# Kernel optimization log

Hardware: AMD Instinct MI355X
Metric: run time of the kernel (lower is better)

## Reference

```python
import jax, jax.numpy as jnp
import numpy as np

B, T, E, D = 64, 512, 1024, 1024  # batch, enc timesteps, enc hidden, dec hidden


def setup_inputs() -> dict:
    key = jax.random.key(0)
    ks = jax.random.split(key, 9)
    s = lambda fan_in: 1.0 / np.sqrt(fan_in)
    return {
        "hidden": jax.random.normal(ks[0], (B, D), jnp.float32),
        "decoder_out": jax.random.normal(ks[1], (B, D), jnp.float32),
        "encoder_states": jax.random.normal(ks[2], (T, B, E), jnp.float32),
        # attn: Linear(D+E -> 2E)
        "Wa": jax.random.uniform(ks[3], (2 * E, D + E), jnp.float32, -s(D + E), s(D + E)),
        "ba": jax.random.uniform(ks[4], (2 * E,), jnp.float32, -s(D + E), s(D + E)),
        # attn2: Linear(2E -> 1)
        "w2": jax.random.uniform(ks[5], (1, 2 * E), jnp.float32, -s(2 * E), s(2 * E)),
        "b2": jax.random.uniform(ks[6], (1,), jnp.float32, -s(2 * E), s(2 * E)),
        # attn_combine: Linear(D+E -> D)
        "Wc": jax.random.uniform(ks[7], (D, D + E), jnp.float32, -s(D + E), s(D + E)),
        "bc": jax.random.uniform(ks[8], (D,), jnp.float32, -s(D + E), s(D + E)),
    }


def reference(hidden, decoder_out, encoder_states, Wa, ba, w2, b2, Wc, bc):
    d = hidden.shape[1]
    # attn(cat(hidden, enc_t)) = hidden @ Wa[:, :D].T + enc_t @ Wa[:, D:].T + ba
    h_proj = hidden @ Wa[:, :d].T + ba                      # [B, 2E]
    e_proj = jnp.einsum('tbe,fe->tbf', encoder_states, Wa[:, d:])  # [T, B, 2E]
    act = jnp.tanh(h_proj[None, :, :] + e_proj)             # [T, B, 2E]
    scores = jnp.einsum('tbf,f->bt', act, w2[0]) + b2[0]    # [B, T]
    weights = jax.nn.softmax(scores, axis=-1)               # softmax over timesteps
    # weighted sum of encoder states: [B, E]
    applied = jnp.einsum('bt,tbe->be', weights, encoder_states)
    combined = jnp.concatenate([decoder_out, applied], axis=1)  # [B, D+E]
    out = jnp.tanh(combined @ Wc.T + bc)                    # [B, D]
    return out, applied
```

## Files before the change

kernel.cpp:

```cpp
#include <hip/hip_runtime.h>
#include <hip/hip_bf16.h>

#define BB 64
#define TT 512
#define EE 1024
#define DD 1024
#define BK 64

typedef __attribute__((ext_vector_type(8))) short s16x8;
typedef __attribute__((ext_vector_type(4))) float f32x4;

#define AS1 __attribute__((address_space(1)))
#define AS3 __attribute__((address_space(3)))

__device__ __forceinline__ float bf2f(unsigned short u) {
    unsigned int x = ((unsigned int)u) << 16;
    return __builtin_bit_cast(float, x);
}
__device__ __forceinline__ unsigned short f2bf(float f) {
    unsigned int u = __builtin_bit_cast(unsigned int, f);
    u += 0x7FFF + ((u >> 16) & 1);
    return (unsigned short)(u >> 16);
}
__device__ __forceinline__ float tanh_fast(float x) {
    x = fminf(fmaxf(x, -15.f), 15.f);
    float e = __expf(2.f * x);
    return (e - 1.f) / (e + 1.f);
}

__device__ __forceinline__ int tile_slot(int row, int g) {
    return (row >> 4) * 128 + (g >> 2) * 64 + (g & 3) * 16 + (row & 15);
}

__global__ __launch_bounds__(256) void conv_encS_kernel(
    const float* __restrict__ enc, unsigned short* __restrict__ encS)
{
    __shared__ short tileL[1024 * 8];
    const int tm  = blockIdx.x;
    const int tk  = blockIdx.y;
    const int tid = threadIdx.x;

#pragma unroll
    for (int it = 0; it < 4; ++it) {
        int cidx = it * 256 + tid;
        int row  = cidx >> 3;
        int g    = cidx & 7;
        const float* src = enc + (size_t)(tm * 128 + row) * 1024 + tk * 64 + g * 8;
        float4 v0 = ((const float4*)src)[0];
        float4 v1 = ((const float4*)src)[1];
        short c[8];
        c[0] = (short)f2bf(v0.x); c[1] = (short)f2bf(v0.y);
        c[2] = (short)f2bf(v0.z); c[3] = (short)f2bf(v0.w);
        c[4] = (short)f2bf(v1.x); c[5] = (short)f2bf(v1.y);
        c[6] = (short)f2bf(v1.z); c[7] = (short)f2bf(v1.w);
        *(s16x8*)&tileL[tile_slot(row, g) * 8] = *(s16x8*)c;
    }
    __syncthreads();
    unsigned short* dst = encS + ((size_t)tm * 16 + tk) * 8192;
#pragma unroll
    for (int it = 0; it < 4; ++it) {
        int s = it * 256 + tid;
        *(s16x8*)&dst[s * 8] = *(const s16x8*)&tileL[s * 8];
    }
}

__global__ __launch_bounds__(256) void conv_waS_kernel(
    const float* __restrict__ Wa, unsigned short* __restrict__ WaS)
{
    __shared__ short tileL[1024 * 8];
    const int tn  = blockIdx.x;
    const int tk  = blockIdx.y;
    const int tid = threadIdx.x;

#pragma unroll
    for (int it = 0; it < 4; ++it) {
        int cidx = it * 256 + tid;
        int row  = cidx >> 3;
        int g    = cidx & 7;
        const float* src = Wa + (size_t)(tn * 128 + row) * 2048 + 1024 + tk * 64 + g * 8;
        float4 v0 = ((const float4*)src)[0];
        float4 v1 = ((const float4*)src)[1];
        short c[8];
        c[0] = (short)f2bf(v0.x); c[1] = (short)f2bf(v0.y);
        c[2] = (short)f2bf(v0.z); c[3] = (short)f2bf(v0.w);
        c[4] = (short)f2bf(v1.x); c[5] = (short)f2bf(v1.y);
        c[6] = (short)f2bf(v1.z); c[7] = (short)f2bf(v1.w);
        *(s16x8*)&tileL[tile_slot(row, g) * 8] = *(s16x8*)c;
    }
    __syncthreads();
    unsigned short* dst = WaS + ((size_t)tn * 16 + tk) * 8192;
#pragma unroll
    for (int it = 0; it < 4; ++it) {
        int s = it * 256 + tid;
        *(s16x8*)&dst[s * 8] = *(const s16x8*)&tileL[s * 8];
    }
}

__global__ __launch_bounds__(256) void hproj_kernel(
    const float* __restrict__ hidden,
    const float* __restrict__ Wa,
    const float* __restrict__ ba,
    float* __restrict__ hp)
{
    __shared__ float sW[8 * 1024];
    const int tid  = threadIdx.x;
    const int lane = tid & 63;
    const int wave = tid >> 6;
    const int f0   = blockIdx.x * 8;

#pragma unroll
    for (int i = 0; i < 8; ++i) {
        int idx = i * 256 + tid;
        int fi  = idx >> 8;
        int c4  = idx & 255;
        ((float4*)sW)[idx] = *(const float4*)(Wa + (size_t)(f0 + fi) * 2048 + c4 * 4);
    }
    __syncthreads();

    for (int bi = 0; bi < 16; ++bi) {
        int b = wave * 16 + bi;
        float h[16];
#pragma unroll
        for (int j = 0; j < 16; ++j) h[j] = hidden[b * 1024 + lane + 64 * j];
#pragma unroll
        for (int fi = 0; fi < 8; ++fi) {
            float s = 0.f;
#pragma unroll
            for (int j = 0; j < 16; ++j) s += h[j] * sW[fi * 1024 + lane + 64 * j];
#pragma unroll
            for (int m = 32; m; m >>= 1) s += __shfl_xor(s, m);
            if (lane == 0) hp[(f0 + fi) * 64 + b] = s + ba[f0 + fi];
        }
    }
}

__global__ __launch_bounds__(512, 2) void gemm_scores(
    const unsigned short* __restrict__ encS,
    const unsigned short* __restrict__ WaS,
    const float* __restrict__ hp,
    const float* __restrict__ w2,
    float* __restrict__ scores)
{
    __shared__ short sA[2][2][8192];
    __shared__ short sB[2][2][8192];
    __shared__ float rowAcc[256];

    const int tid  = threadIdx.x;
    const int bid  = blockIdx.x;
    const int w    = (bid & 7) * 128 + (bid >> 3);
    const int bm   = w >> 3;
    const int bn   = w & 7;
    const int lane = tid & 63;
    const int wave = tid >> 6;
    const int wm   = wave >> 2;
    const int wn   = wave & 3;
    const int c    = lane & 15;
    const int quad = lane >> 4;
    const int ntile = wn >> 1;
    const int nrow0 = (wn & 1) * 4;

    f32x4 acc[8][4];
#pragma unroll
    for (int m = 0; m < 8; ++m)
#pragma unroll
        for (int n = 0; n < 4; ++n)
#pragma unroll
            for (int r = 0; r < 4; ++r) acc[m][n][r] = 0.f;

    const unsigned short* aT = encS + ((size_t)(bm * 2) * 16) * 8192;
    const unsigned short* bT = WaS  + ((size_t)(bn * 2) * 16) * 8192;

    auto STAGE_PAIR = [&](int kt, int nb, int p) {
        if (p < 2) {
            const unsigned short* src = aT + ((size_t)(p * 16 + kt)) * 8192;
            __builtin_amdgcn_global_load_lds(
                (const AS1 void*)(src + tid * 8),
                (AS3 void*)&sA[nb][p][tid * 8], 16, 0, 0);
            __builtin_amdgcn_global_load_lds(
                (const AS1 void*)(src + (512 + tid) * 8),
                (AS3 void*)&sA[nb][p][(512 + tid) * 8], 16, 0, 0);
        } else {
            const int nt = p - 2;
            const unsigned short* src = bT + ((size_t)(nt * 16 + kt)) * 8192;
            __builtin_amdgcn_global_load_lds(
                (const AS1 void*)(src + tid * 8),
                (AS3 void*)&sB[nb][nt][tid * 8], 16, 0, 0);
            __builtin_amdgcn_global_load_lds(
                (const AS1 void*)(src + (512 + tid) * 8),
                (AS3 void*)&sB[nb][nt][(512 + tid) * 8], 16, 0, 0);
        }
    };

#pragma unroll
    for (int p = 0; p < 4; ++p) STAGE_PAIR(0, 0, p);

    for (int kt = 0; kt < 16; ++kt) {
        const int cur = kt & 1;
        asm volatile("s_waitcnt vmcnt(0)" ::: "memory");
        __builtin_amdgcn_s_barrier();
        __builtin_amdgcn_sched_barrier(0);
        const bool pf = (kt < 15);

        s16x8 bF[2][4];
#pragma unroll
        for (int p = 0; p < 4; ++p) {
            if (p == 0) {
#pragma unroll
                for (int n = 0; n < 4; ++n)
#pragma unroll
                    for (int kk = 0; kk < 2; ++kk)
                        bF[kk][n] = *(const s16x8*)
                            &sB[cur][ntile][((nrow0 + n) * 128 + kk * 64 + lane) * 8];
            }
            s16x8 aF[2][2];
#pragma unroll
            for (int j = 0; j < 2; ++j)
#pragma unroll
                for (int kk = 0; kk < 2; ++kk)
                    aF[j][kk] = *(const s16x8*)
                        &sA[cur][wm][((2 * p + j) * 128 + kk * 64 + lane) * 8];

            if (pf) STAGE_PAIR(kt + 1, cur ^ 1, p);

            __builtin_amdgcn_sched_barrier(0);
            __builtin_amdgcn_s_barrier();
            __builtin_amdgcn_s_setprio(1);
#pragma unroll
            for (int j = 0; j < 2; ++j)
#pragma unroll
                for (int kk = 0; kk < 2; ++kk)
#pragma unroll
                    for (int n = 0; n < 4; ++n)
                        acc[2 * p + j][n] = __builtin_amdgcn_mfma_f32_16x16x32_bf16(
                            aF[j][kk], bF[kk][n], acc[2 * p + j][n], 0, 0, 0);
            __builtin_amdgcn_s_setprio(0);
            __builtin_amdgcn_sched_barrier(0);
            if (p < 3) __builtin_amdgcn_s_barrier();
        }
    }

    __syncthreads();
    if (tid < 256) rowAcc[tid] = 0.f;
    __syncthreads();

    float w2v[4];
#pragma unroll
    for (int n = 0; n < 4; ++n) w2v[n] = w2[bn * 256 + wn * 64 + n * 16 + c];

#pragma unroll
    for (int m = 0; m < 8; ++m) {
        int lrow0 = wm * 128 + m * 16 + quad * 4;
        int b0    = lrow0 & 63;
        f32x4 hp4[4];
#pragma unroll
        for (int n = 0; n < 4; ++n)
            hp4[n] = *(const f32x4*)&hp[(bn * 256 + wn * 64 + n * 16 + c) * 64 + b0];
#pragma unroll
        for (int r = 0; r < 4; ++r) {
            float s = 0.f;
#pragma unroll
            for (int n = 0; n < 4; ++n)
                s += tanh_fast(acc[m][n][r] + hp4[n][r]) * w2v[n];
            s += __shfl_xor(s, 1);
            s += __shfl_xor(s, 2);
            s += __shfl_xor(s, 4);
            s += __shfl_xor(s, 8);
            if (c == 0) atomicAdd(&rowAcc[lrow0 + r], s);
        }
    }
    __syncthreads();
    if (tid < 256) {
        int b = tid & 63;
        int t = bm * 4 + (tid >> 6);
        atomicAdd(&scores[b * TT + t], rowAcc[tid]);
    }
}

__global__ __launch_bounds__(256) void softmax_kernel(float* __restrict__ scores)
{
    __shared__ float wmax[4];
    __shared__ float wsum[4];
    const int b   = blockIdx.x;
    const int tid = threadIdx.x;
    float* row = scores + b * TT;

    float v0 = row[tid], v1 = row[tid + 256];
    float m = fmaxf(v0, v1);
#pragma unroll
    for (int s = 32; s; s >>= 1) m = fmaxf(m, __shfl_xor(m, s));
    if ((tid & 63) == 0) wmax[tid >> 6] = m;
    __syncthreads();
    m = fmaxf(fmaxf(wmax[0], wmax[1]), fmaxf(wmax[2], wmax[3]));

    float e0 = __expf(v0 - m), e1 = __expf(v1 - m);
    float s = e0 + e1;
#pragma unroll
    for (int t = 32; t; t >>= 1) s += __shfl_xor(s, t);
    if ((tid & 63) == 0) wsum[tid >> 6] = s;
    __syncthreads();
    float inv = 1.f / (wsum[0] + wsum[1] + wsum[2] + wsum[3]);
    row[tid]       = e0 * inv;
    row[tid + 256] = e1 * inv;
}

__global__ __launch_bounds__(256) void applied_part_kernel(
    const float* __restrict__ enc,
    const float* __restrict__ w,
    float* __restrict__ part)
{
    __shared__ float red[128 * 8];
    const int tc  = blockIdx.x;
    const int b   = blockIdx.y;
    const int tid = threadIdx.x;
    const int eo  = tid & 127;
    const int th  = tid >> 7;
    const int e0  = eo * 8;

    float a[8];
#pragma unroll
    for (int j = 0; j < 8; ++j) a[j] = 0.f;

    for (int it = 0; it < 16; ++it) {
        int t = tc * 32 + th * 16 + it;
        float wt = w[b * TT + t];
        const float* src = enc + ((size_t)(t * BB + b)) * EE + e0;
        float4 v0 = ((const float4*)src)[0];
        float4 v1 = ((const float4*)src)[1];
        a[0] += wt * v0.x; a[1] += wt * v0.y; a[2] += wt * v0.z; a[3] += wt * v0.w;
        a[4] += wt * v1.x; a[5] += wt * v1.y; a[6] += wt * v1.z; a[7] += wt * v1.w;
    }
    if (th == 1) {
#pragma unroll
        for (int j = 0; j < 8; ++j) red[eo * 8 + j] = a[j];
    }
    __syncthreads();
    if (th == 0) {
        float* dst = part + ((size_t)tc * 64 + b) * 1024 + e0;
#pragma unroll
        for (int j = 0; j < 8; ++j) dst[j] = a[j] + red[eo * 8 + j];
    }
}

__global__ __launch_bounds__(256) void applied_reduce_kernel(
    const float* __restrict__ part, float* __restrict__ out_applied)
{
    int idx = blockIdx.x * 256 + threadIdx.x;
    float s = 0.f;
#pragma unroll
    for (int tc = 0; tc < 16; ++tc) s += part[tc * 65536 + idx];
    out_applied[idx] = s;
}

__global__ __launch_bounds__(256) void combine_kernel(
    const float* __restrict__ dec,
    const float* applied,
    const float* __restrict__ Wc,
    const float* __restrict__ bc,
    float* out0)
{
    const int gw   = blockIdx.x * 4 + (threadIdx.x >> 6);
    const int lane = threadIdx.x & 63;
    const int d0   = (gw >> 3) * 8;
    const int b0   = (gw & 7) * 8;

    float acc[8][8];
#pragma unroll
    for (int dd = 0; dd < 8; ++dd)
#pragma unroll
        for (int bb = 0; bb < 8; ++bb) acc[dd][bb] = 0.f;

#pragma unroll
    for (int j = 0; j < 8; ++j) {
        float4 wv[8];
#pragma unroll
        for (int dd = 0; dd < 8; ++dd)
            wv[dd] = ((const float4*)(Wc + (size_t)(d0 + dd) * 2048))[j * 64 + lane];
        float4 cv[8];
        if (j < 4) {
#pragma unroll
            for (int bb = 0; bb < 8; ++bb)
                cv[bb] = ((const float4*)(dec + (size_t)(b0 + bb) * 1024))[j * 64 + lane];
        } else {
#pragma unroll
            for (int bb = 0; bb < 8; ++bb)
                cv[bb] = ((const float4*)(applied + (size_t)(b0 + bb) * 1024))[(j - 4) * 64 + lane];
        }
#pragma unroll
        for (int dd = 0; dd < 8; ++dd)
#pragma unroll
            for (int bb = 0; bb < 8; ++bb)
                acc[dd][bb] += wv[dd].x * cv[bb].x + wv[dd].y * cv[bb].y
                             + wv[dd].z * cv[bb].z + wv[dd].w * cv[bb].w;
    }

#pragma unroll
    for (int dd = 0; dd < 8; ++dd) {
#pragma unroll
        for (int bb = 0; bb < 8; ++bb) {
            float s = acc[dd][bb];
#pragma unroll
            for (int m = 32; m; m >>= 1) s += __shfl_xor(s, m);
            if (lane == 0)
                out0[(size_t)(b0 + bb) * DD + d0 + dd] = tanh_fast(s + bc[d0 + dd]);
        }
    }
}

extern "C" void kernel_launch(void* const* d_in, const int* in_sizes, int n_in,
                              void* d_out, int out_size, void* d_ws, size_t ws_size,
                              hipStream_t stream) {
    const float* hidden = (const float*)d_in[0];
    const float* dec    = (const float*)d_in[1];
    const float* enc    = (const float*)d_in[2];
    const float* Wa     = (const float*)d_in[3];
    const float* ba     = (const float*)d_in[4];
    const float* w2     = (const float*)d_in[5];
    const float* Wc     = (const float*)d_in[7];
    const float* bc     = (const float*)d_in[8];
    float* out = (float*)d_out;

    unsigned short* encS = (unsigned short*)d_ws;
    unsigned short* WaS  = encS + (size_t)33554432;
    float* hp     = (float*)(WaS + (size_t)2097152);
    float* scores = hp + 131072;
    float* part   = scores + 32768;

    hipMemsetAsync(scores, 0, BB * TT * sizeof(float), stream);
    dim3 gc(256, 16);
    conv_encS_kernel<<<gc, 256, 0, stream>>>(enc, encS);
    dim3 gw(16, 16);
    conv_waS_kernel<<<gw, 256, 0, stream>>>(Wa, WaS);
    hproj_kernel<<<256, 256, 0, stream>>>(hidden, Wa, ba, hp);
    gemm_scores<<<1024, 512, 0, stream>>>(encS, WaS, hp, w2, scores);
    softmax_kernel<<<BB, 256, 0, stream>>>(scores);
    dim3 g3(16, 64);
    applied_part_kernel<<<g3, 256, 0, stream>>>(enc, scores, part);
    applied_reduce_kernel<<<256, 256, 0, stream>>>(part, out + BB * DD);
    combine_kernel<<<256, 256, 0, stream>>>(dec, out + BB * DD, Wc, bc, out);
}
```

Before: 609.8 us.

## Use 1024-thread blocks in scores GEMM with 4x4 per-wave tiles

The scores GEMM now launches 16 waves per block instead of 8, so each wave owns a 64x64 sub-tile (4x4 MFMA accumulators) rather than 128x64. The per-phase staging/compute interleave with extra barriers is replaced by issuing the whole next-k prefetch at the start of each k-step, followed by two kk sub-steps of fragment loads and MFMAs. This halves accumulator registers per wave and cuts barrier count, aiming for more latency hiding. In exchange, each block has more waves contending for LDS, and occupancy drops to one block per CU, so overlap of loads with compute within a block becomes more important.

```diff
diff --git a/kernel.cpp b/kernel.cpp
--- a/kernel.cpp
+++ b/kernel.cpp
@@ -134,7 +134,7 @@
     }
 }
 
-__global__ __launch_bounds__(512, 2) void gemm_scores(
+__global__ __launch_bounds__(1024) void gemm_scores(
     const unsigned short* __restrict__ encS,
     const unsigned short* __restrict__ WaS,
     const float* __restrict__ hp,
@@ -156,12 +156,14 @@
     const int wn   = wave & 3;
     const int c    = lane & 15;
     const int quad = lane >> 4;
-    const int ntile = wn >> 1;
+    const int mt   = wm >> 1;
+    const int mrow0 = (wm & 1) * 4;
+    const int nt   = wn >> 1;
     const int nrow0 = (wn & 1) * 4;
 
-    f32x4 acc[8][4];
-#pragma unroll
-    for (int m = 0; m < 8; ++m)
+    f32x4 acc[4][4];
+#pragma unroll
+    for (int m = 0; m < 4; ++m)
 #pragma unroll
         for (int n = 0; n < 4; ++n)
 #pragma unroll
@@ -170,76 +172,54 @@
     const unsigned short* aT = encS + ((size_t)(bm * 2) * 16) * 8192;
     const unsigned short* bT = WaS  + ((size_t)(bn * 2) * 16) * 8192;
 
-    auto STAGE_PAIR = [&](int kt, int nb, int p) {
-        if (p < 2) {
-            const unsigned short* src = aT + ((size_t)(p * 16 + kt)) * 8192;
+    auto STAGE_ALL = [&](int kt, int nb) {
+#pragma unroll
+        for (int t = 0; t < 2; ++t) {
+            const unsigned short* sa = aT + ((size_t)(t * 16 + kt)) * 8192;
             __builtin_amdgcn_global_load_lds(
-                (const AS1 void*)(src + tid * 8),
-                (AS3 void*)&sA[nb][p][tid * 8], 16, 0, 0);
+                (const AS1 void*)(sa + tid * 8),
+                (AS3 void*)&sA[nb][t][tid * 8], 16, 0, 0);
+            const unsigned short* sb = bT + ((size_t)(t * 16 + kt)) * 8192;
             __builtin_amdgcn_global_load_lds(
-                (const AS1 void*)(src + (512 + tid) * 8),
-                (AS3 void*)&sA[nb][p][(512 + tid) * 8], 16, 0, 0);
-        } else {
-            const int nt = p - 2;
-            const unsigned short* src = bT + ((size_t)(nt * 16 + kt)) * 8192;
-            __builtin_amdgcn_global_load_lds(
-                (const AS1 void*)(src + tid * 8),
-                (AS3 void*)&sB[nb][nt][tid * 8], 16, 0, 0);
-            __builtin_amdgcn_global_load_lds(
-                (const AS1 void*)(src + (512 + tid) * 8),
-                (AS3 void*)&sB[nb][nt][(512 + tid) * 8], 16, 0, 0);
+                (const AS1 void*)(sb + tid * 8),
+                (AS3 void*)&sB[nb][t][tid * 8], 16, 0, 0);
         }
     };
 
-#pragma unroll
-    for (int p = 0; p < 4; ++p) STAGE_PAIR(0, 0, p);
+    STAGE_ALL(0, 0);
 
     for (int kt = 0; kt < 16; ++kt) {
         const int cur = kt & 1;
         asm volatile("s_waitcnt vmcnt(0)" ::: "memory");
         __builtin_amdgcn_s_barrier();
         __builtin_amdgcn_sched_barrier(0);
-        const bool pf = (kt < 15);
-
-        s16x8 bF[2][4];
-#pragma unroll
-        for (int p = 0; p < 4; ++p) {
-            if (p == 0) {
+        if (kt < 15) STAGE_ALL(kt + 1, cur ^ 1);
+
+#pragma unroll
+        for (int kk = 0; kk < 2; ++kk) {
+            s16x8 aF[4], bF[4];
+#pragma unroll
+            for (int m = 0; m < 4; ++m)
+                aF[m] = *(const s16x8*)
+                    &sA[cur][mt][((mrow0 + m) * 128 + kk * 64 + lane) * 8];
+#pragma unroll
+            for (int n = 0; n < 4; ++n)
+                bF[n] = *(const s16x8*)
+                    &sB[cur][nt][((nrow0 + n) * 128 + kk * 64 + lane) * 8];
+
+            __builtin_amdgcn_s_setprio(1);
+#pragma unroll
+            for (int m = 0; m < 4; ++m)
 #pragma unroll
                 for (int n = 0; n < 4; ++n)
-#pragma unroll
-                    for (int kk = 0; kk < 2; ++kk)
-                        bF[kk][n] = *(const s16x8*)
-                            &sB[cur][ntile][((nrow0 + n) * 128 + kk * 64 + lane) * 8];
-            }
-            s16x8 aF[2][2];
-#pragma unroll
-            for (int j = 0; j < 2; ++j)
-#pragma unroll
-                for (int kk = 0; kk < 2; ++kk)
-                    aF[j][kk] = *(const s16x8*)
-                        &sA[cur][wm][((2 * p + j) * 128 + kk * 64 + lane) * 8];
-
-            if (pf) STAGE_PAIR(kt + 1, cur ^ 1, p);
-
-            __builtin_amdgcn_sched_barrier(0);
-            __builtin_amdgcn_s_barrier();
-            __builtin_amdgcn_s_setprio(1);
-#pragma unroll
-            for (int j = 0; j < 2; ++j)
-#pragma unroll
-                for (int kk = 0; kk < 2; ++kk)
-#pragma unroll
-                    for (int n = 0; n < 4; ++n)
-                        acc[2 * p + j][n] = __builtin_amdgcn_mfma_f32_16x16x32_bf16(
-                            aF[j][kk], bF[kk][n], acc[2 * p + j][n], 0, 0, 0);
+                    acc[m][n] = __builtin_amdgcn_mfma_f32_16x16x32_bf16(
+                        aF[m], bF[n], acc[m][n], 0, 0, 0);
             __builtin_amdgcn_s_setprio(0);
-            __builtin_amdgcn_sched_barrier(0);
-            if (p < 3) __builtin_amdgcn_s_barrier();
-        }
-    }
-
-    __syncthreads();
+        }
+        __builtin_amdgcn_sched_barrier(0);
+        __builtin_amdgcn_s_barrier();
+    }
+
     if (tid < 256) rowAcc[tid] = 0.f;
     __syncthreads();
 
@@ -248,8 +228,8 @@
     for (int n = 0; n < 4; ++n) w2v[n] = w2[bn * 256 + wn * 64 + n * 16 + c];
 
 #pragma unroll
-    for (int m = 0; m < 8; ++m) {
-        int lrow0 = wm * 128 + m * 16 + quad * 4;
+    for (int m = 0; m < 4; ++m) {
+        int lrow0 = wm * 64 + m * 16 + quad * 4;
         int b0    = lrow0 & 63;
         f32x4 hp4[4];
 #pragma unroll
@@ -431,7 +411,7 @@
     dim3 gw(16, 16);
     conv_waS_kernel<<<gw, 256, 0, stream>>>(Wa, WaS);
     hproj_kernel<<<256, 256, 0, stream>>>(hidden, Wa, ba, hp);
-    gemm_scores<<<1024, 512, 0, stream>>>(encS, WaS, hp, w2, scores);
+    gemm_scores<<<1024, 1024, 0, stream>>>(encS, WaS, hp, w2, scores);
     softmax_kernel<<<BB, 256, 0, stream>>>(scores);
     dim3 g3(16, 64);
     applied_part_kernel<<<g3, 256, 0, stream>>>(enc, scores, part);
```

Result: faster. 511.8 us (-16.1%).
